# Performance work log

Hardware: AMD Instinct MI355X
Metric: run time of the kernel (lower is better)

## Reference

```python
import jax, jax.numpy as jnp
import numpy as np

HIDDEN = 1024
H = 16        # query heads
HK = 4        # kv heads
G = H // HK   # GQA group size
D = 64        # head dim
EPS = 1e-6


def rmsnorm(x, w):
    # normalize over last dim (head_dim)
    var = jnp.mean(jnp.square(x), axis=-1, keepdims=True)
    return x * jax.lax.rsqrt(var + EPS) * w


def setup_inputs() -> dict:
    key = jax.random.key(0)
    ks = jax.random.split(key, 8)
    B, S_KV, S_Q = 2, 4096, 512
    inputs = jax.random.normal(ks[0], (B, S_KV, HIDDEN), dtype=jnp.float32)
    latent = jax.random.normal(ks[1], (B, S_Q, HIDDEN), dtype=jnp.float32)
    # xavier_uniform-style init: limit = sqrt(6/(fan_in+fan_out))
    def xavier(k, shape, gain=1.0):
        fan_out, fan_in = shape
        limit = gain * np.sqrt(6.0 / (fan_in + fan_out))
        return jax.random.uniform(k, shape, jnp.float32, -limit, limit)
    wq = xavier(ks[2], (H * D, HIDDEN))
    wk = xavier(ks[3], (HK * D, HIDDEN))
    wv = xavier(ks[4], (HK * D, HIDDEN))
    wo = xavier(ks[5], (HIDDEN, H * D), gain=1.0 / np.sqrt(2.0))
    q_norm_w = jnp.ones((D,), jnp.float32)
    k_norm_w = jnp.ones((D,), jnp.float32)
    return {"inputs": inputs, "latent": latent, "wq": wq, "wk": wk,
            "wv": wv, "wo": wo, "q_norm_w": q_norm_w, "k_norm_w": k_norm_w}


def reference(inputs, latent, wq, wk, wv, wo, q_norm_w, k_norm_w):
    B, S_q, _ = latent.shape
    S_kv = inputs.shape[1]
    # projections (Linear: x @ W^T)
    q = (latent @ wq.T).reshape(B, S_q, H, D)    # [B,Sq,H,D]
    k = (inputs @ wk.T).reshape(B, S_kv, HK, D)  # [B,Skv,Hk,D]
    v = (inputs @ wv.T).reshape(B, S_kv, HK, D)
    q = rmsnorm(q, q_norm_w)
    k = rmsnorm(k, k_norm_w)
    # GQA without materializing repeated K/V: view q as [B,Hk,G,Sq,D]
    q = q.transpose(0, 2, 1, 3).reshape(B, HK, G, S_q, D)
    k = k.transpose(0, 2, 1, 3)  # [B,Hk,Skv,D]
    v = v.transpose(0, 2, 1, 3)  # [B,Hk,Skv,D]
    # NOTE: no 1/sqrt(D) scaling, faithful to the source module
    scores = jnp.einsum('bkgqd,bksd->bkgqs', q, k)  # [B,Hk,G,Sq,Skv]
    attn = jax.nn.softmax(scores.astype(jnp.float32), axis=-1).astype(q.dtype)
    out = jnp.einsum('bkgqs,bksd->bkgqd', attn, v)  # [B,Hk,G,Sq,D]
    # back to [B,Sq,H*D]
    out = out.reshape(B, H, S_q, D).transpose(0, 2, 1, 3).reshape(B, S_q, H * D)
    return out @ wo.T
```

## Files before the change

### kernel.cpp

```cpp
#include <hip/hip_runtime.h>

#define NB 2
#define SQ 512
#define SKV 4096
#define HID 1024
#define NH 16
#define NHK 4
#define NG 4
#define HD 64
#define EPSF 1e-6f
#define NSPLIT 4
#define RB (NB * NH * SQ)

typedef short v8s __attribute__((ext_vector_type(8)));
typedef short v4s __attribute__((ext_vector_type(4)));
typedef float v4f __attribute__((ext_vector_type(4)));
typedef float v2f __attribute__((ext_vector_type(2)));

static __device__ __forceinline__ short f2bf(float f) {
  unsigned u = __builtin_bit_cast(unsigned, f);
  u += 0x7FFFu + ((u >> 16) & 1u);
  return (short)(u >> 16);
}

static __device__ __forceinline__ v8s lds_frag(const short* lds, int row, int kbyte) {
  return *(const v8s*)((const char*)lds + row * 128 + (kbyte ^ ((row & 7) << 4)));
}

template<int SRC_F32, int NIT>
static __device__ __forceinline__ void stage_tile(const void* src, int ld,
                                                  int r0, int c0, short* lds, int t) {
#pragma unroll
  for (int i = 0; i < NIT; ++i) {
    int flat = t * 8 + i * 2048;
    int row = flat >> 6, col = flat & 63;
    v8s v;
    if (SRC_F32) {
      const float* p = (const float*)src + (size_t)(r0 + row) * ld + c0 + col;
      v4f a = *(const v4f*)p;
      v4f b = *(const v4f*)(p + 4);
      v[0] = f2bf(a[0]); v[1] = f2bf(a[1]); v[2] = f2bf(a[2]); v[3] = f2bf(a[3]);
      v[4] = f2bf(b[0]); v[5] = f2bf(b[1]); v[6] = f2bf(b[2]); v[7] = f2bf(b[3]);
    } else {
      v = *(const v8s*)((const short*)src + (size_t)(r0 + row) * ld + c0 + col);
    }
    *(v8s*)((char*)lds + row * 128 + ((col * 2) ^ ((row & 7) << 4))) = v;
  }
}

__global__ __launch_bounds__(256) void proj_kv(const float* __restrict__ A,
                                               const float* __restrict__ Wk,
                                               const float* __restrict__ Wv,
                                               const float* __restrict__ knw,
                                               short* __restrict__ Kb,
                                               short* __restrict__ Vtb) {
  __shared__ __align__(16) short Asm[128 * 64];
  __shared__ __align__(16) short Bsm[128 * 64];
  const int t = threadIdx.x, lane = t & 63, w = t >> 6;
  const int l15 = lane & 15, g4 = lane >> 4;
  const int wr = w >> 1, wc = w & 1;
  const int m0 = blockIdx.x * 128, n0 = blockIdx.y * 128;
  const int isV = blockIdx.z;
  const float* W = isV ? Wv : Wk;
  v4f acc[4][4] = {};
  for (int k0 = 0; k0 < HID; k0 += 64) {
    __syncthreads();
    stage_tile<1, 4>(A, HID, m0, k0, Asm, t);
    stage_tile<1, 4>(W, HID, n0, k0, Bsm, t);
    __syncthreads();
    v8s af[4][2], bfr[4][2];
#pragma unroll
    for (int mf = 0; mf < 4; ++mf)
#pragma unroll
      for (int s = 0; s < 2; ++s)
        af[mf][s] = lds_frag(Asm, wr * 64 + mf * 16 + l15, s * 64 + g4 * 16);
#pragma unroll
    for (int nf = 0; nf < 4; ++nf)
#pragma unroll
      for (int s = 0; s < 2; ++s)
        bfr[nf][s] = lds_frag(Bsm, wc * 64 + nf * 16 + l15, s * 64 + g4 * 16);
#pragma unroll
    for (int mf = 0; mf < 4; ++mf)
#pragma unroll
      for (int nf = 0; nf < 4; ++nf)
#pragma unroll
        for (int s = 0; s < 2; ++s)
          acc[mf][nf] = __builtin_amdgcn_mfma_f32_16x16x32_bf16(af[mf][s], bfr[nf][s],
                                                                acc[mf][nf], 0, 0, 0);
  }
  const int head = blockIdx.y * 2 + wc;
  if (!isV) {
    float wcol[4];
#pragma unroll
    for (int nf = 0; nf < 4; ++nf) wcol[nf] = knw[nf * 16 + l15];
#pragma unroll
    for (int mf = 0; mf < 4; ++mf)
#pragma unroll
      for (int j = 0; j < 4; ++j) {
        float ss = acc[mf][0][j] * acc[mf][0][j] + acc[mf][1][j] * acc[mf][1][j] +
                   acc[mf][2][j] * acc[mf][2][j] + acc[mf][3][j] * acc[mf][3][j];
#pragma unroll
        for (int msk = 1; msk < 16; msk <<= 1) ss += __shfl_xor(ss, msk);
        float sc = rsqrtf(ss * (1.0f / 64.0f) + EPSF);
        int m = m0 + wr * 64 + mf * 16 + g4 * 4 + j;
        int b = m >> 12, sl = m & (SKV - 1);
        size_t base = ((size_t)(b * NHK + head) * SKV + sl) * 64;
#pragma unroll
        for (int nf = 0; nf < 4; ++nf)
          Kb[base + nf * 16 + l15] = f2bf(acc[mf][nf][j] * sc * wcol[nf]);
      }
  } else {
#pragma unroll
    for (int mf = 0; mf < 4; ++mf) {
      int m = m0 + wr * 64 + mf * 16 + g4 * 4;
      int b = m >> 12, sl = m & (SKV - 1);
#pragma unroll
      for (int nf = 0; nf < 4; ++nf) {
        int d = nf * 16 + l15;
        v4s o;
#pragma unroll
        for (int j = 0; j < 4; ++j) o[j] = f2bf(acc[mf][nf][j]);
        *(v4s*)(Vtb + ((size_t)(b * NHK + head) * 64 + d) * SKV + sl) = o;
      }
    }
  }
}

template<int KIND>
__global__ __launch_bounds__(256) void gemm64(const void* __restrict__ Ap,
                                              const float* __restrict__ W,
                                              const float* __restrict__ wn,
                                              void* __restrict__ outp) {
  __shared__ __align__(16) short Asm[64 * 64];
  __shared__ __align__(16) short Bsm[128 * 64];
  const int t = threadIdx.x, lane = t & 63, w = t >> 6;
  const int l15 = lane & 15, g4 = lane >> 4;
  const int wr = w >> 1, wc = w & 1;
  const int m0 = blockIdx.x * 64, n0 = blockIdx.y * 128;
  v4f acc[2][4] = {};
  for (int k0 = 0; k0 < HID; k0 += 64) {
    __syncthreads();
    stage_tile<(KIND == 0) ? 1 : 0, 2>(Ap, HID, m0, k0, Asm, t);
    stage_tile<1, 4>(W, HID, n0, k0, Bsm, t);
    __syncthreads();
    v8s af[2][2], bfr[4][2];
#pragma unroll
    for (int mf = 0; mf < 2; ++mf)
#pragma unroll
      for (int s = 0; s < 2; ++s)
        af[mf][s] = lds_frag(Asm, wr * 32 + mf * 16 + l15, s * 64 + g4 * 16);
#pragma unroll
    for (int nf = 0; nf < 4; ++nf)
#pragma unroll
      for (int s = 0; s < 2; ++s)
        bfr[nf][s] = lds_frag(Bsm, wc * 64 + nf * 16 + l15, s * 64 + g4 * 16);
#pragma unroll
    for (int mf = 0; mf < 2; ++mf)
#pragma unroll
      for (int nf = 0; nf < 4; ++nf)
#pragma unroll
        for (int s = 0; s < 2; ++s)
          acc[mf][nf] = __builtin_amdgcn_mfma_f32_16x16x32_bf16(af[mf][s], bfr[nf][s],
                                                                acc[mf][nf], 0, 0, 0);
  }
  if (KIND == 0) {
    short* outb = (short*)outp;
    const int head = blockIdx.y * 2 + wc;
    float wcol[4];
#pragma unroll
    for (int nf = 0; nf < 4; ++nf) wcol[nf] = wn[nf * 16 + l15];
#pragma unroll
    for (int mf = 0; mf < 2; ++mf)
#pragma unroll
      for (int j = 0; j < 4; ++j) {
        float ss = acc[mf][0][j] * acc[mf][0][j] + acc[mf][1][j] * acc[mf][1][j] +
                   acc[mf][2][j] * acc[mf][2][j] + acc[mf][3][j] * acc[mf][3][j];
#pragma unroll
        for (int msk = 1; msk < 16; msk <<= 1) ss += __shfl_xor(ss, msk);
        float sc = rsqrtf(ss * (1.0f / 64.0f) + EPSF);
        int m = m0 + wr * 32 + mf * 16 + g4 * 4 + j;
        int b = m >> 9, sl = m & (SQ - 1);
        size_t base = ((size_t)(b * NH + head) * SQ + sl) * 64;
#pragma unroll
        for (int nf = 0; nf < 4; ++nf)
          outb[base + nf * 16 + l15] = f2bf(acc[mf][nf][j] * sc * wcol[nf]);
      }
  } else {
    float* C = (float*)outp;
#pragma unroll
    for (int mf = 0; mf < 2; ++mf)
#pragma unroll
      for (int j = 0; j < 4; ++j) {
        int m = m0 + wr * 32 + mf * 16 + g4 * 4 + j;
#pragma unroll
        for (int nf = 0; nf < 4; ++nf)
          C[(size_t)m * HID + n0 + wc * 64 + nf * 16 + l15] = acc[mf][nf][j];
      }
  }
}

__global__ __launch_bounds__(256) void attn_kernel(const short* __restrict__ Qb,
                                                   const short* __restrict__ Kb,
                                                   const short* __restrict__ Vt,
                                                   float* __restrict__ Op,
                                                   float* __restrict__ Ml) {
  __shared__ __align__(16) short Ksm[2][64 * 64];
  __shared__ __align__(16) short Vsm[2][64 * 64];
  __shared__ __align__(16) short Psm[4][16 * 64];
  int id = blockIdx.x;
  int qt = id & 31, hk = (id >> 5) & 3, b = (id >> 7) & 1, sp = id >> 8;
  int t = threadIdx.x, w = t >> 6, lane = t & 63;
  int l15 = lane & 15, g4 = lane >> 4;
  int h = hk * NG + w;

  const short* qbase = Qb + (((size_t)(b * NH + h)) * SQ + qt * 16) * 64;
  v8s aq[2];
#pragma unroll
  for (int s = 0; s < 2; ++s)
    aq[s] = *(const v8s*)(qbase + (size_t)l15 * 64 + s * 32 + g4 * 8);

  const short* kbase = Kb + ((size_t)(b * NHK + hk)) * SKV * 64;
  const short* vbase = Vt + ((size_t)(b * NHK + hk)) * 64 * SKV;
  char* pbase = (char*)&Psm[w][0];

  v4f acco[4] = {};
  float mrow[4], lrow[4];
#pragma unroll
  for (int r = 0; r < 4; ++r) { mrow[r] = -__builtin_inff(); lrow[r] = 0.f; }

  const int KV0 = sp * (SKV / NSPLIT);
  for (int kt = 0; kt < SKV / NSPLIT / 128; ++kt) {
    int kv0 = KV0 + kt * 128;
    __syncthreads();
    stage_tile<0, 2>(kbase, 64, kv0, 0, Ksm[0], t);
    stage_tile<0, 2>(kbase, 64, kv0 + 64, 0, Ksm[1], t);
    stage_tile<0, 2>(vbase, SKV, 0, kv0, Vsm[0], t);
    stage_tile<0, 2>(vbase, SKV, 0, kv0 + 64, Vsm[1], t);
    __syncthreads();

    v4f accs[8] = {};
#pragma unroll
    for (int hf = 0; hf < 2; ++hf)
#pragma unroll
      for (int f = 0; f < 4; ++f)
#pragma unroll
        for (int s = 0; s < 2; ++s) {
          v8s bk = lds_frag(Ksm[hf], f * 16 + l15, s * 64 + g4 * 16);
          accs[hf * 4 + f] =
              __builtin_amdgcn_mfma_f32_16x16x32_bf16(aq[s], bk, accs[hf * 4 + f], 0, 0, 0);
        }

    float tm[4];
#pragma unroll
    for (int r = 0; r < 4; ++r) {
      float m01 = fmaxf(accs[0][r], accs[1][r]), m23 = fmaxf(accs[2][r], accs[3][r]);
      float m45 = fmaxf(accs[4][r], accs[5][r]), m67 = fmaxf(accs[6][r], accs[7][r]);
      tm[r] = fmaxf(fmaxf(m01, m23), fmaxf(m45, m67));
    }
#pragma unroll
    for (int msk = 1; msk < 16; msk <<= 1)
#pragma unroll
      for (int r = 0; r < 4; ++r)
        tm[r] = fmaxf(tm[r], __shfl_xor(tm[r], msk));
    float al[4];
#pragma unroll
    for (int r = 0; r < 4; ++r) {
      float mn = fmaxf(mrow[r], tm[r]);
      al[r] = __expf(mrow[r] - mn);
      mrow[r] = mn;
    }
    float rs[4] = {0.f, 0.f, 0.f, 0.f};
#pragma unroll
    for (int f = 0; f < 8; ++f)
#pragma unroll
      for (int r = 0; r < 4; ++r) {
        accs[f][r] = __expf(accs[f][r] - mrow[r]);
        rs[r] += accs[f][r];
      }
#pragma unroll
    for (int msk = 1; msk < 16; msk <<= 1)
#pragma unroll
      for (int r = 0; r < 4; ++r) rs[r] += __shfl_xor(rs[r], msk);
#pragma unroll
    for (int r = 0; r < 4; ++r) lrow[r] = lrow[r] * al[r] + rs[r];
#pragma unroll
    for (int fd = 0; fd < 4; ++fd)
#pragma unroll
      for (int r = 0; r < 4; ++r) acco[fd][r] *= al[r];

#pragma unroll
    for (int hf = 0; hf < 2; ++hf) {
#pragma unroll
      for (int f = 0; f < 4; ++f)
#pragma unroll
        for (int r = 0; r < 4; ++r) {
          int row = g4 * 4 + r;
          int colB = (f * 16 + l15) * 2;
          *(short*)(pbase + row * 128 + (colB ^ ((row & 7) << 4))) = f2bf(accs[hf * 4 + f][r]);
        }
      asm volatile("s_waitcnt lgkmcnt(0)" ::: "memory");
      __builtin_amdgcn_sched_barrier(0);
      v8s pa[2];
#pragma unroll
      for (int s = 0; s < 2; ++s)
        pa[s] = *(const v8s*)(pbase + l15 * 128 + ((s * 64 + g4 * 16) ^ ((l15 & 7) << 4)));
      asm volatile("s_waitcnt lgkmcnt(0)" ::: "memory");
      __builtin_amdgcn_sched_barrier(0);
#pragma unroll
      for (int fd = 0; fd < 4; ++fd)
#pragma unroll
        for (int s = 0; s < 2; ++s) {
          v8s vb = lds_frag(Vsm[hf], fd * 16 + l15, s * 64 + g4 * 16);
          acco[fd] = __builtin_amdgcn_mfma_f32_16x16x32_bf16(pa[s], vb, acco[fd], 0, 0, 0);
        }
    }
  }

  size_t rowbase = ((size_t)b * NH + h) * SQ + qt * 16;
#pragma unroll
  for (int fd = 0; fd < 4; ++fd)
#pragma unroll
    for (int r = 0; r < 4; ++r) {
      int row = g4 * 4 + r;
      Op[((size_t)sp * RB + rowbase + row) * 64 + fd * 16 + l15] = acco[fd][r];
    }
  if (l15 == 0) {
#pragma unroll
    for (int r = 0; r < 4; ++r) {
      int row = g4 * 4 + r;
      v2f ml; ml[0] = mrow[r]; ml[1] = lrow[r];
      *(v2f*)(Ml + ((size_t)sp * RB + rowbase + row) * 2) = ml;
    }
  }
}

__global__ __launch_bounds__(256) void merge_attn(const float* __restrict__ Op,
                                                  const float* __restrict__ Ml,
                                                  short* __restrict__ Ab) {
  int idx = blockIdx.x * 256 + threadIdx.x;
  int d = idx & 63, row = idx >> 6;
  float ms[NSPLIT], ls[NSPLIT];
  float M = -__builtin_inff();
#pragma unroll
  for (int s = 0; s < NSPLIT; ++s) {
    v2f ml = *(const v2f*)(Ml + ((size_t)s * RB + row) * 2);
    ms[s] = ml[0]; ls[s] = ml[1];
    M = fmaxf(M, ms[s]);
  }
  float L = 0.f, o = 0.f;
#pragma unroll
  for (int s = 0; s < NSPLIT; ++s) {
    float wgt = __expf(ms[s] - M);
    L += ls[s] * wgt;
    o += wgt * Op[((size_t)s * RB + row) * 64 + d];
  }
  int b = row >> 13;
  int hh = (row >> 9) & 15;
  int sq = row & 511;
  Ab[((size_t)(b * SQ + sq)) * HID + hh * 64 + d] = f2bf(o / L);
}

extern "C" void kernel_launch(void* const* d_in, const int* in_sizes, int n_in,
                              void* d_out, int out_size, void* d_ws, size_t ws_size,
                              hipStream_t stream) {
  const float* inputs = (const float*)d_in[0];
  const float* latent = (const float*)d_in[1];
  const float* wq = (const float*)d_in[2];
  const float* wk = (const float*)d_in[3];
  const float* wv = (const float*)d_in[4];
  const float* wo = (const float*)d_in[5];
  const float* qnw = (const float*)d_in[6];
  const float* knw = (const float*)d_in[7];

  char* ws = (char*)d_ws;
  float* Op  = (float*)(ws);
  float* Ml  = (float*)(ws + 16777216);
  short* Qb  = (short*)(ws + 17825792);
  short* Kb  = (short*)(ws + 19922944);
  short* Vtb = (short*)(ws + 24117248);
  short* Ab  = (short*)(ws + 28311552);

  gemm64<0><<<dim3(16, 8), 256, 0, stream>>>(latent, wq, qnw, Qb);
  proj_kv<<<dim3(64, 2, 2), 256, 0, stream>>>(inputs, wk, wv, knw, Kb, Vtb);
  attn_kernel<<<256 * NSPLIT, 256, 0, stream>>>(Qb, Kb, Vtb, Op, Ml);
  merge_attn<<<RB * 64 / 256, 256, 0, stream>>>(Op, Ml, Ab);
  gemm64<1><<<dim3(16, 8), 256, 0, stream>>>(Ab, wo, nullptr, (float*)d_out);
}
```

Before: 240.8 us.

## Merge Q/K/V projections into one launch and split-K the output projection

Combines the Q projection and the K/V projection into a single kernel with 640 blocks. The K/V tiles shrink to one head (64 columns), so the grid grows from 256 to 512 blocks. The output projection is split into four K-slices that write fp32 partials into the workspace, followed by a reduction kernel. f2bf now uses the native __bf16 conversion. The aim is to fill more CUs on these small GEMMs (the old launches had 128 or 256 blocks) and to drop one launch. In exchange, the input activation tile is staged more times per block, and the split-K adds partial-sum traffic and an extra kernel.

Result: faster. 232.8 us (-3.3%).

```diff
diff --git a/kernel.cpp b/kernel.cpp
--- a/kernel.cpp
+++ b/kernel.cpp
@@ -18,9 +18,8 @@
 typedef float v2f __attribute__((ext_vector_type(2)));
 
 static __device__ __forceinline__ short f2bf(float f) {
-  unsigned u = __builtin_bit_cast(unsigned, f);
-  u += 0x7FFFu + ((u >> 16) & 1u);
-  return (short)(u >> 16);
+  __bf16 b = (__bf16)f;
+  return (short)__builtin_bit_cast(unsigned short, b);
 }
 
 static __device__ __forceinline__ v8s lds_frag(const short* lds, int row, int kbyte) {
@@ -48,53 +47,123 @@
   }
 }
 
-__global__ __launch_bounds__(256) void proj_kv(const float* __restrict__ A,
-                                               const float* __restrict__ Wk,
-                                               const float* __restrict__ Wv,
-                                               const float* __restrict__ knw,
-                                               short* __restrict__ Kb,
-                                               short* __restrict__ Vtb) {
+__global__ __launch_bounds__(256) void proj_all(const float* __restrict__ inputs,
+                                                const float* __restrict__ latent,
+                                                const float* __restrict__ wq,
+                                                const float* __restrict__ wk,
+                                                const float* __restrict__ wv,
+                                                const float* __restrict__ qnw,
+                                                const float* __restrict__ knw,
+                                                short* __restrict__ Qb,
+                                                short* __restrict__ Kb,
+                                                short* __restrict__ Vtb) {
   __shared__ __align__(16) short Asm[128 * 64];
   __shared__ __align__(16) short Bsm[128 * 64];
+  const int bid = blockIdx.x;
   const int t = threadIdx.x, lane = t & 63, w = t >> 6;
   const int l15 = lane & 15, g4 = lane >> 4;
-  const int wr = w >> 1, wc = w & 1;
-  const int m0 = blockIdx.x * 128, n0 = blockIdx.y * 128;
-  const int isV = blockIdx.z;
-  const float* W = isV ? Wv : Wk;
-  v4f acc[4][4] = {};
-  for (int k0 = 0; k0 < HID; k0 += 64) {
-    __syncthreads();
-    stage_tile<1, 4>(A, HID, m0, k0, Asm, t);
-    stage_tile<1, 4>(W, HID, n0, k0, Bsm, t);
-    __syncthreads();
-    v8s af[4][2], bfr[4][2];
-#pragma unroll
-    for (int mf = 0; mf < 4; ++mf)
-#pragma unroll
-      for (int s = 0; s < 2; ++s)
-        af[mf][s] = lds_frag(Asm, wr * 64 + mf * 16 + l15, s * 64 + g4 * 16);
-#pragma unroll
-    for (int nf = 0; nf < 4; ++nf)
-#pragma unroll
-      for (int s = 0; s < 2; ++s)
-        bfr[nf][s] = lds_frag(Bsm, wc * 64 + nf * 16 + l15, s * 64 + g4 * 16);
-#pragma unroll
-    for (int mf = 0; mf < 4; ++mf)
+  v4f acc[2][4] = {};
+
+  if (bid < 512) {
+    const int z = bid & 1, head = (bid >> 1) & 3, mblk = bid >> 3;
+    const int m0 = mblk * 128;
+    const float* W = z ? wv : wk;
+    for (int k0 = 0; k0 < HID; k0 += 64) {
+      __syncthreads();
+      stage_tile<1, 4>(inputs, HID, m0, k0, Asm, t);
+      stage_tile<1, 2>(W, HID, head * 64, k0, Bsm, t);
+      __syncthreads();
+      v8s af[2][2], bfr[4][2];
+#pragma unroll
+      for (int mf = 0; mf < 2; ++mf)
+#pragma unroll
+        for (int s = 0; s < 2; ++s)
+          af[mf][s] = lds_frag(Asm, w * 32 + mf * 16 + l15, s * 64 + g4 * 16);
 #pragma unroll
       for (int nf = 0; nf < 4; ++nf)
 #pragma unroll
         for (int s = 0; s < 2; ++s)
-          acc[mf][nf] = __builtin_amdgcn_mfma_f32_16x16x32_bf16(af[mf][s], bfr[nf][s],
-                                                                acc[mf][nf], 0, 0, 0);
-  }
-  const int head = blockIdx.y * 2 + wc;
-  if (!isV) {
+          bfr[nf][s] = lds_frag(Bsm, nf * 16 + l15, s * 64 + g4 * 16);
+#pragma unroll
+      for (int mf = 0; mf < 2; ++mf)
+#pragma unroll
+        for (int nf = 0; nf < 4; ++nf)
+#pragma unroll
+          for (int s = 0; s < 2; ++s)
+            acc[mf][nf] = __builtin_amdgcn_mfma_f32_16x16x32_bf16(af[mf][s], bfr[nf][s],
+                                                                  acc[mf][nf], 0, 0, 0);
+    }
+    if (!z) {
+      float wcol[4];
+#pragma unroll
+      for (int nf = 0; nf < 4; ++nf) wcol[nf] = knw[nf * 16 + l15];
+#pragma unroll
+      for (int mf = 0; mf < 2; ++mf)
+#pragma unroll
+        for (int j = 0; j < 4; ++j) {
+          float ss = acc[mf][0][j] * acc[mf][0][j] + acc[mf][1][j] * acc[mf][1][j] +
+                     acc[mf][2][j] * acc[mf][2][j] + acc[mf][3][j] * acc[mf][3][j];
+#pragma unroll
+          for (int msk = 1; msk < 16; msk <<= 1) ss += __shfl_xor(ss, msk);
+          float sc = rsqrtf(ss * (1.0f / 64.0f) + EPSF);
+          int m = m0 + w * 32 + mf * 16 + g4 * 4 + j;
+          int b = m >> 12, sl = m & (SKV - 1);
+          size_t base = ((size_t)(b * NHK + head) * SKV + sl) * 64;
+#pragma unroll
+          for (int nf = 0; nf < 4; ++nf)
+            Kb[base + nf * 16 + l15] = f2bf(acc[mf][nf][j] * sc * wcol[nf]);
+        }
+    } else {
+#pragma unroll
+      for (int mf = 0; mf < 2; ++mf) {
+        int m = m0 + w * 32 + mf * 16 + g4 * 4;
+        int b = m >> 12, sl = m & (SKV - 1);
+#pragma unroll
+        for (int nf = 0; nf < 4; ++nf) {
+          int d = nf * 16 + l15;
+          v4s o;
+#pragma unroll
+          for (int j = 0; j < 4; ++j) o[j] = f2bf(acc[mf][nf][j]);
+          *(v4s*)(Vtb + ((size_t)(b * NHK + head) * 64 + d) * SKV + sl) = o;
+        }
+      }
+    }
+  } else {
+    const int r = bid - 512;
+    const int mblk = r & 15, nblk = r >> 4;
+    const int m0 = mblk * 64;
+    const int wr = w >> 1, wc = w & 1;
+    for (int k0 = 0; k0 < HID; k0 += 64) {
+      __syncthreads();
+      stage_tile<1, 2>(latent, HID, m0, k0, Asm, t);
+      stage_tile<1, 4>(wq, HID, nblk * 128, k0, Bsm, t);
+      __syncthreads();
+      v8s af[2][2], bfr[4][2];
+#pragma unroll
+      for (int mf = 0; mf < 2; ++mf)
+#pragma unroll
+        for (int s = 0; s < 2; ++s)
+          af[mf][s] = lds_frag(Asm, wr * 32 + mf * 16 + l15, s * 64 + g4 * 16);
+#pragma unroll
+      for (int nf = 0; nf < 4; ++nf)
+#pragma unroll
+        for (int s = 0; s < 2; ++s)
+          bfr[nf][s] = lds_frag(Bsm, wc * 64 + nf * 16 + l15, s * 64 + g4 * 16);
+#pragma unroll
+      for (int mf = 0; mf < 2; ++mf)
+#pragma unroll
+        for (int nf = 0; nf < 4; ++nf)
+#pragma unroll
+          for (int s = 0; s < 2; ++s)
+            acc[mf][nf] = __builtin_amdgcn_mfma_f32_16x16x32_bf16(af[mf][s], bfr[nf][s],
+                                                                  acc[mf][nf], 0, 0, 0);
+    }
+    const int head = nblk * 2 + wc;
     float wcol[4];
 #pragma unroll
-    for (int nf = 0; nf < 4; ++nf) wcol[nf] = knw[nf * 16 + l15];
-#pragma unroll
-    for (int mf = 0; mf < 4; ++mf)
+    for (int nf = 0; nf < 4; ++nf) wcol[nf] = qnw[nf * 16 + l15];
+#pragma unroll
+    for (int mf = 0; mf < 2; ++mf)
 #pragma unroll
       for (int j = 0; j < 4; ++j) {
         float ss = acc[mf][0][j] * acc[mf][0][j] + acc[mf][1][j] * acc[mf][1][j] +
@@ -102,46 +171,31 @@
 #pragma unroll
         for (int msk = 1; msk < 16; msk <<= 1) ss += __shfl_xor(ss, msk);
         float sc = rsqrtf(ss * (1.0f / 64.0f) + EPSF);
-        int m = m0 + wr * 64 + mf * 16 + g4 * 4 + j;
-        int b = m >> 12, sl = m & (SKV - 1);
-        size_t base = ((size_t)(b * NHK + head) * SKV + sl) * 64;
+        int m = m0 + wr * 32 + mf * 16 + g4 * 4 + j;
+        int b = m >> 9, sl = m & (SQ - 1);
+        size_t base = ((size_t)(b * NH + head) * SQ + sl) * 64;
 #pragma unroll
         for (int nf = 0; nf < 4; ++nf)
-          Kb[base + nf * 16 + l15] = f2bf(acc[mf][nf][j] * sc * wcol[nf]);
+          Qb[base + nf * 16 + l15] = f2bf(acc[mf][nf][j] * sc * wcol[nf]);
       }
-  } else {
-#pragma unroll
-    for (int mf = 0; mf < 4; ++mf) {
-      int m = m0 + wr * 64 + mf * 16 + g4 * 4;
-      int b = m >> 12, sl = m & (SKV - 1);
-#pragma unroll
-      for (int nf = 0; nf < 4; ++nf) {
-        int d = nf * 16 + l15;
-        v4s o;
-#pragma unroll
-        for (int j = 0; j < 4; ++j) o[j] = f2bf(acc[mf][nf][j]);
-        *(v4s*)(Vtb + ((size_t)(b * NHK + head) * 64 + d) * SKV + sl) = o;
-      }
-    }
-  }
-}
-
-template<int KIND>
-__global__ __launch_bounds__(256) void gemm64(const void* __restrict__ Ap,
-                                              const float* __restrict__ W,
-                                              const float* __restrict__ wn,
-                                              void* __restrict__ outp) {
+  }
+}
+
+__global__ __launch_bounds__(256) void wo_gemm(const short* __restrict__ Ab,
+                                               const float* __restrict__ Wo,
+                                               float* __restrict__ Wop) {
   __shared__ __align__(16) short Asm[64 * 64];
   __shared__ __align__(16) short Bsm[128 * 64];
   const int t = threadIdx.x, lane = t & 63, w = t >> 6;
   const int l15 = lane & 15, g4 = lane >> 4;
   const int wr = w >> 1, wc = w & 1;
-  const int m0 = blockIdx.x * 64, n0 = blockIdx.y * 128;
+  const int m0 = blockIdx.x * 64, n0 = blockIdx.y * 128, ks = blockIdx.z;
   v4f acc[2][4] = {};
-  for (int k0 = 0; k0 < HID; k0 += 64) {
+  for (int kk = 0; kk < 4; ++kk) {
+    int k0 = ks * 256 + kk * 64;
     __syncthreads();
-    stage_tile<(KIND == 0) ? 1 : 0, 2>(Ap, HID, m0, k0, Asm, t);
-    stage_tile<1, 4>(W, HID, n0, k0, Bsm, t);
+    stage_tile<0, 2>(Ab, HID, m0, k0, Asm, t);
+    stage_tile<1, 4>(Wo, HID, n0, k0, Bsm, t);
     __syncthreads();
     v8s af[2][2], bfr[4][2];
 #pragma unroll
@@ -163,40 +217,28 @@
           acc[mf][nf] = __builtin_amdgcn_mfma_f32_16x16x32_bf16(af[mf][s], bfr[nf][s],
                                                                 acc[mf][nf], 0, 0, 0);
   }
-  if (KIND == 0) {
-    short* outb = (short*)outp;
-    const int head = blockIdx.y * 2 + wc;
-    float wcol[4];
-#pragma unroll
-    for (int nf = 0; nf < 4; ++nf) wcol[nf] = wn[nf * 16 + l15];
-#pragma unroll
-    for (int mf = 0; mf < 2; ++mf)
-#pragma unroll
-      for (int j = 0; j < 4; ++j) {
-        float ss = acc[mf][0][j] * acc[mf][0][j] + acc[mf][1][j] * acc[mf][1][j] +
-                   acc[mf][2][j] * acc[mf][2][j] + acc[mf][3][j] * acc[mf][3][j];
-#pragma unroll
-        for (int msk = 1; msk < 16; msk <<= 1) ss += __shfl_xor(ss, msk);
-        float sc = rsqrtf(ss * (1.0f / 64.0f) + EPSF);
-        int m = m0 + wr * 32 + mf * 16 + g4 * 4 + j;
-        int b = m >> 9, sl = m & (SQ - 1);
-        size_t base = ((size_t)(b * NH + head) * SQ + sl) * 64;
-#pragma unroll
-        for (int nf = 0; nf < 4; ++nf)
-          outb[base + nf * 16 + l15] = f2bf(acc[mf][nf][j] * sc * wcol[nf]);
-      }
-  } else {
-    float* C = (float*)outp;
-#pragma unroll
-    for (int mf = 0; mf < 2; ++mf)
-#pragma unroll
-      for (int j = 0; j < 4; ++j) {
-        int m = m0 + wr * 32 + mf * 16 + g4 * 4 + j;
-#pragma unroll
-        for (int nf = 0; nf < 4; ++nf)
-          C[(size_t)m * HID + n0 + wc * 64 + nf * 16 + l15] = acc[mf][nf][j];
-      }
-  }
+  float* C = Wop + (size_t)ks * HID * NB * SQ;
+#pragma unroll
+  for (int mf = 0; mf < 2; ++mf)
+#pragma unroll
+    for (int j = 0; j < 4; ++j) {
+      int m = m0 + wr * 32 + mf * 16 + g4 * 4 + j;
+#pragma unroll
+      for (int nf = 0; nf < 4; ++nf)
+        C[(size_t)m * HID + n0 + wc * 64 + nf * 16 + l15] = acc[mf][nf][j];
+    }
+}
+
+__global__ __launch_bounds__(256) void wo_reduce(const float* __restrict__ Wop,
+                                                 float* __restrict__ out) {
+  int idx = (blockIdx.x * 256 + threadIdx.x) * 4;
+  v4f s = *(const v4f*)(Wop + idx);
+#pragma unroll
+  for (int ks = 1; ks < 4; ++ks) {
+    v4f p = *(const v4f*)(Wop + (size_t)ks * HID * NB * SQ + idx);
+    s[0] += p[0]; s[1] += p[1]; s[2] += p[2]; s[3] += p[3];
+  }
+  *(v4f*)(out + idx) = s;
 }
 
 __global__ __launch_bounds__(256) void attn_kernel(const short* __restrict__ Qb,
@@ -374,15 +416,16 @@
 
   char* ws = (char*)d_ws;
   float* Op  = (float*)(ws);
+  float* Wop = (float*)(ws);
   float* Ml  = (float*)(ws + 16777216);
   short* Qb  = (short*)(ws + 17825792);
   short* Kb  = (short*)(ws + 19922944);
   short* Vtb = (short*)(ws + 24117248);
   short* Ab  = (short*)(ws + 28311552);
 
-  gemm64<0><<<dim3(16, 8), 256, 0, stream>>>(latent, wq, qnw, Qb);
-  proj_kv<<<dim3(64, 2, 2), 256, 0, stream>>>(inputs, wk, wv, knw, Kb, Vtb);
+  proj_all<<<640, 256, 0, stream>>>(inputs, latent, wq, wk, wv, qnw, knw, Qb, Kb, Vtb);
   attn_kernel<<<256 * NSPLIT, 256, 0, stream>>>(Qb, Kb, Vtb, Op, Ml);
   merge_attn<<<RB * 64 / 256, 256, 0, stream>>>(Op, Ml, Ab);
-  gemm64<1><<<dim3(16, 8), 256, 0, stream>>>(Ab, wo, nullptr, (float*)d_out);
-}
+  wo_gemm<<<dim3(16, 8, 4), 256, 0, stream>>>(Ab, wo, Wop);
+  wo_reduce<<<1024, 256, 0, stream>>>(Wop, (float*)d_out);
+}
```
